# Optimization experiments

Measured on AMD Instinct MI355X. Metric: run time of the kernel, lower is better.

The kernel has to match this reference:

```python
import jax, jax.numpy as jnp
import numpy as np

N = 8192   # points
C = 64     # feature planes (planes[0])
H = 4      # num_heads
K = 16     # nsample (KNN neighbors)
DH = C // H
EPS = 1e-9


def setup_inputs() -> dict:
    key = jax.random.key(0)
    ks = jax.random.split(key, 13)
    w = lambda k, sh: jax.random.normal(k, sh, jnp.float32) * 0.05
    p = jax.random.normal(ks[0], (N, 3), jnp.float32)
    nrm = jax.random.normal(ks[1], (N, 3), jnp.float32)
    normals = nrm / jnp.sqrt(jnp.sum(nrm * nrm, -1, keepdims=True) + EPS)
    x = jax.random.normal(ks[2], (N, C), jnp.float32)
    return {
        "p": p, "x": x, "normals": normals,
        "Wq": w(ks[3], (C, C)), "Wk": w(ks[4], (C, C)), "Wv": w(ks[5], (C, C)),
        "Wo": w(ks[6], (C, C)),
        "ppf_w1": w(ks[7], (4, C)), "ppf_b1": jnp.zeros((C,), jnp.float32),
        "ppf_w2": w(ks[8], (C, C)), "ppf_b2": jnp.zeros((C,), jnp.float32),
        "ln_g": jnp.ones((C,), jnp.float32), "ln_b": jnp.zeros((C,), jnp.float32),
    }


def _angle(u, v):
    # rotation-invariant angle via atan2(||u x v||, u . v); eps keeps grads finite at 0
    cr = jnp.cross(u, v)
    return jnp.arctan2(jnp.sqrt(jnp.sum(cr * cr, -1) + EPS), jnp.sum(u * v, -1))


def reference(p, x, normals, Wq, Wk, Wv, Wo, ppf_w1, ppf_b1, ppf_w2, ppf_b2, ln_g, ln_b):
    # --- KNN grouping (pointops.queryandgroup equivalent) ---
    sq = jnp.sum(p * p, -1)
    d2 = sq[:, None] + sq[None, :] - 2.0 * (p @ p.T)   # (N,N) pairwise sq dists
    _, idx = jax.lax.top_k(-d2, K)                      # (N,K) neighbor indices

    # --- PPF features (calc_ppf_gpu) ---
    p_r = p[idx]                                        # (N,K,3)
    n_r = normals[idx]                                  # (N,K,3)
    d = p_r - p[:, None, :]
    nc = jnp.broadcast_to(normals[:, None, :], d.shape)
    ppf = jnp.stack([
        _angle(nc, d),
        _angle(n_r, d),
        _angle(nc, n_r),
        jnp.sqrt(jnp.sum(d * d, -1) + EPS),
    ], -1)                                              # (N,K,4)

    # --- LocalPPFTransformer: PPF-conditioned local multi-head attention ---
    pe = jax.nn.relu(ppf @ ppf_w1 + ppf_b1) @ ppf_w2 + ppf_b2   # (N,K,C)
    q = (x @ Wq).reshape(N, H, DH)
    xg = x[idx]                                                  # (N,K,C) gather
    k = (xg @ Wk + pe).reshape(N, K, H, DH)
    v = (xg @ Wv + pe).reshape(N, K, H, DH)
    scale = 1.0 / np.sqrt(DH).astype(np.float32)
    attn = jax.nn.softmax(jnp.einsum('nhd,nkhd->nhk', q, k) * scale, axis=-1)
    out = jnp.einsum('nhk,nkhd->nhd', attn, v).reshape(N, C) @ Wo

    # --- block tail: LayerNorm, residual, ReLU ---
    mu = jnp.mean(out, -1, keepdims=True)
    var = jnp.var(out, -1, keepdims=True)
    out = (out - mu) * jax.lax.rsqrt(var + 1e-5) * ln_g + ln_b
    return jax.nn.relu(out + x)
```

## Files before the change

kernel.cpp:

```cpp
#include <hip/hip_runtime.h>
#include <hip/hip_bf16.h>
#include <math.h>

#define N_PTS 8192
#define QPW 4
#define LCAP 192
#define KNN_BLOCKS (N_PTS / 4)

#define OFF_W2 0
#define OFF_WO 4096
#define OFF_WQB 8192
#define OFF_WKB 12288
#define OFF_WVB 16384
#define PACK_N 20480
#define PREP_BLOCKS (N_PTS / 256)
#define PACK_BLOCKS ((PACK_N + 255) / 256)

typedef __hip_bfloat16 bf16;
typedef __attribute__((ext_vector_type(8))) short short8;
typedef __attribute__((ext_vector_type(4))) float floatx4;

#define INFF __int_as_float(0x7f800000)

__device__ __forceinline__ float ldf(const float* p, int i) { return p[i]; }
__device__ __forceinline__ float ldf(const bf16* p, int i) { return __bfloat162float(p[i]); }
__device__ __forceinline__ void stf(float* p, int i, float v) { p[i] = v; }
__device__ __forceinline__ void stf(bf16* p, int i, float v) { p[i] = __float2bfloat16(v); }

__device__ __forceinline__ unsigned short f2bfbits(float x) {
    bf16 h = __float2bfloat16(x);
    return *reinterpret_cast<unsigned short*>(&h);
}
__device__ __forceinline__ float bfbits2f(unsigned short u) {
    bf16 h;
    *reinterpret_cast<unsigned short*>(&h) = u;
    return __bfloat162float(h);
}

__device__ __forceinline__ short8 load_xfrag(const bf16* x, int row, int off) {
    return *(const short8*)((const unsigned short*)x + row * 64 + off);
}
__device__ __forceinline__ short8 load_xfrag(const float* x, int row, int off) {
    short8 v;
#pragma unroll
    for (int i = 0; i < 8; ++i) v[i] = (short)f2bfbits(x[row * 64 + off + i]);
    return v;
}

__device__ __forceinline__ bool is_bf16(const void* g) {
    return *(const unsigned int*)g != 0x3F800000u;
}

template <typename T>
__device__ __forceinline__ void prep_pack_body(const T* p, float4* p4,
                                               const T* w2, const T* Wo,
                                               const T* Wq, const T* Wk,
                                               const T* Wv,
                                               unsigned short* pack) {
    if (blockIdx.x < PREP_BLOCKS) {
        int i = blockIdx.x * 256 + threadIdx.x;
        float x = ldf(p, 3 * i + 0);
        float y = ldf(p, 3 * i + 1);
        float z = ldf(p, 3 * i + 2);
        p4[i] = make_float4(x, y, z, 0.5f * (x * x + y * y + z * z));
        return;
    }
    int i = (blockIdx.x - PREP_BLOCKS) * 256 + threadIdx.x;
    if (i >= PACK_N) return;
    if (i >= OFF_WO && i < OFF_WQB) {
        int j = i - OFF_WO, t = j >> 6, c = j & 63;
        pack[i] = f2bfbits(ldf(Wo, c * 64 + t));
    } else {
        const T* W = (i < OFF_WO) ? w2
                     : (i < OFF_WKB ? Wq : (i < OFF_WVB ? Wk : Wv));
        int j = i & 4095;
        int ii = j & 7, lane = (j >> 3) & 63, frag = j >> 9;
        int tile = frag >> 1, s = frag & 1, g = lane >> 4, m16 = lane & 15;
        int k = s * 32 + g * 8 + ii, n = tile * 16 + m16;
        pack[i] = f2bfbits(ldf(W, k * 64 + n));
    }
}
__global__ __launch_bounds__(256) void prep_pack_kernel(
    const void* p, float4* p4, const void* w2, const void* Wo, const void* Wq,
    const void* Wk, const void* Wv, unsigned short* pack, const void* gref) {
    if (is_bf16(gref))
        prep_pack_body<bf16>((const bf16*)p, p4, (const bf16*)w2,
                             (const bf16*)Wo, (const bf16*)Wq, (const bf16*)Wk,
                             (const bf16*)Wv, pack);
    else
        prep_pack_body<float>((const float*)p, p4, (const float*)w2,
                              (const float*)Wo, (const float*)Wq,
                              (const float*)Wk, (const float*)Wv, pack);
}

__global__ __launch_bounds__(256, 8) void knn_kernel(
    const float4* __restrict__ p4, unsigned short* __restrict__ nbrs_g) {
    __shared__ unsigned long long list[QPW][LCAP];
    __shared__ float Tw_sh[QPW][4];
    __shared__ unsigned int cnt[QPW];
    __shared__ int nbrs[QPW][16];

    const int tid = threadIdx.x;
    const int lane = tid & 63;
    const int wave = tid >> 6;
    const int qbase = blockIdx.x * QPW;
    const int cbase = wave * (N_PTS / 4);

    float4 c[QPW];
#pragma unroll
    for (int q = 0; q < QPW; ++q) c[q] = p4[qbase + q];

    if (tid < QPW) cnt[tid] = 0;

    float lmin[QPW];
#pragma unroll
    for (int q = 0; q < QPW; ++q) lmin[q] = INFF;

#pragma unroll 4
    for (int it = 0; it < N_PTS / 4 / 64; ++it) {
        float4 pj = p4[cbase + it * 64 + lane];
#pragma unroll
        for (int q = 0; q < QPW; ++q) {
            float f = fmaf(-c[q].x, pj.x,
                      fmaf(-c[q].y, pj.y, fmaf(-c[q].z, pj.z, pj.w)));
            lmin[q] = fminf(lmin[q], f);
        }
    }

#pragma unroll
    for (int q = 0; q < QPW; ++q) {
        float v = lmin[q];
#pragma unroll
        for (int k = 2; k <= 64; k <<= 1) {
#pragma unroll
            for (int j = k >> 1; j >= 1; j >>= 1) {
                float o = __shfl_xor(v, j, 64);
                bool keepmin = (((lane & k) == 0) == ((lane & j) == 0));
                v = keepmin ? fminf(v, o) : fmaxf(v, o);
            }
        }
        float Tw = __shfl(v, 15, 64);
        if (lane == 0) Tw_sh[q][wave] = Tw;
    }
    __syncthreads();

    float T[QPW];
#pragma unroll
    for (int q = 0; q < QPW; ++q)
        T[q] = fminf(fminf(Tw_sh[q][0], Tw_sh[q][1]),
                     fminf(Tw_sh[q][2], Tw_sh[q][3]));

#pragma unroll 2
    for (int it = 0; it < N_PTS / 4 / 64; ++it) {
        int j = cbase + it * 64 + lane;
        float4 pj = p4[j];
#pragma unroll
        for (int q = 0; q < QPW; ++q) {
            float f = fmaf(-c[q].x, pj.x,
                      fmaf(-c[q].y, pj.y, fmaf(-c[q].z, pj.z, pj.w)));
            bool sel = f <= T[q];
            unsigned long long ball = __ballot(sel);
            if (ball) {
                int leader = (int)__ffsll((long long)ball) - 1;
                unsigned int base = 0;
                if (lane == leader)
                    base = atomicAdd(&cnt[q], (unsigned int)__popcll(ball));
                base = (unsigned int)__shfl((int)base, leader, 64);
                if (sel) {
                    unsigned int bits = __float_as_uint(f);
                    bits ^= (unsigned int)(((int)bits >> 31)) | 0x80000000u;
                    unsigned long long key =
                        ((unsigned long long)bits << 32) | (unsigned int)j;
                    unsigned int mb =
                        __builtin_amdgcn_mbcnt_lo((unsigned int)ball, 0u);
                    mb = __builtin_amdgcn_mbcnt_hi((unsigned int)(ball >> 32),
                                                   mb);
                    unsigned int pos = base + mb;
                    if (pos < LCAP) list[q][pos] = key;
                }
            }
        }
    }
    __syncthreads();

    {
        const int q = wave;
        int m = cnt[q] < (unsigned)LCAP ? (int)cnt[q] : LCAP;
#pragma unroll
        for (int s = 0; s < LCAP / 64; ++s) {
            int idx = lane + s * 64;
            if (idx < m) {
                unsigned long long k = list[q][idx];
                int r = 0;
#pragma unroll 1
                for (int e = 0; e < m; ++e) r += (list[q][e] < k);
                if (r < 16) nbrs[q][r] = (int)(k & 0xFFFFFFFFu);
            }
        }
    }
    __syncthreads();

    if (tid < QPW * 16)
        nbrs_g[qbase * 16 + tid] =
            (unsigned short)((const int*)nbrs)[tid];
}

__device__ __forceinline__ float angle3(float ux, float uy, float uz, float vx,
                                        float vy, float vz) {
    float cx = uy * vz - uz * vy;
    float cy = uz * vx - ux * vz;
    float cz = ux * vy - uy * vx;
    float cn = sqrtf(cx * cx + cy * cy + cz * cz + 1e-9f);
    float d = ux * vx + uy * vy + uz * vz;
    return atan2f(cn, d);
}

template <typename T>
__device__ __forceinline__ void attn4_body(
    int n, int t, const float4* p4, const T* normals, const T* w1, const T* b1,
    const T* b2, const unsigned short* pack, const T* x, const T* ln_g,
    const T* ln_b, T* out, const unsigned short* nbr, float* scr,
    unsigned short (*kh)[72], unsigned short (*vbuf)[72]) {
    const int m16 = t & 15, g = t >> 4;

    float w10 = ldf(w1, 0 * 64 + t);
    float w11 = ldf(w1, 1 * 64 + t);
    float w12 = ldf(w1, 2 * 64 + t);
    float w13 = ldf(w1, 3 * 64 + t);
    float bb1 = ldf(b1, t);
    float b2c[4];
#pragma unroll
    for (int tile = 0; tile < 4; ++tile) b2c[tile] = ldf(b2, tile * 16 + m16);

    {
        int k = t >> 2, f = t & 3;
        int j = nbr[k];
        float4 pc = p4[n];
        float4 pj = p4[j];
        float dx = pj.x - pc.x, dy = pj.y - pc.y, dz = pj.z - pc.z;
        float v;
        if (f == 3) {
            v = sqrtf(dx * dx + dy * dy + dz * dz + 1e-9f);
        } else if (f == 0) {
            float ncx = ldf(normals, n * 3 + 0);
            float ncy = ldf(normals, n * 3 + 1);
            float ncz = ldf(normals, n * 3 + 2);
            v = angle3(ncx, ncy, ncz, dx, dy, dz);
        } else if (f == 1) {
            float njx = ldf(normals, j * 3 + 0);
            float njy = ldf(normals, j * 3 + 1);
            float njz = ldf(normals, j * 3 + 2);
            v = angle3(njx, njy, njz, dx, dy, dz);
        } else {
            float ncx = ldf(normals, n * 3 + 0);
            float ncy = ldf(normals, n * 3 + 1);
            float ncz = ldf(normals, n * 3 + 2);
            float njx = ldf(normals, j * 3 + 0);
            float njy = ldf(normals, j * 3 + 1);
            float njz = ldf(normals, j * 3 + 2);
            v = angle3(ncx, ncy, ncz, njx, njy, njz);
        }
        scr[t] = v;
    }
    __syncthreads();

    {
        const float4* pp = (const float4*)scr;
#pragma unroll
        for (int k = 0; k < 16; ++k) {
            float4 pf = pp[k];
            float h = fmaf(pf.w, w13,
                      fmaf(pf.z, w12, fmaf(pf.y, w11, fmaf(pf.x, w10, bb1))));
            kh[k][t] = f2bfbits(fmaxf(h, 0.0f));
        }
    }
    __syncthreads();

    short8 afr[2];
#pragma unroll
    for (int s = 0; s < 2; ++s)
        afr[s] = *(const short8*)&kh[m16][g * 8 + s * 32];

    short8 axfr[2], qfr[2];
#pragma unroll
    for (int s = 0; s < 2; ++s) {
        axfr[s] = load_xfrag(x, nbr[m16], g * 8 + s * 32);
        qfr[s] = load_xfrag(x, n, g * 8 + s * 32);
    }

    float qreg = 0.f;
    {
        const short8* pw2 = (const short8*)(pack + OFF_W2);
        const short8* pwq = (const short8*)(pack + OFF_WQB);
        const short8* pwk = (const short8*)(pack + OFF_WKB);
        const short8* pwv = (const short8*)(pack + OFF_WVB);
#pragma unroll
        for (int tile = 0; tile < 4; ++tile) {
            floatx4 accp = (floatx4){0.f, 0.f, 0.f, 0.f};
            accp = __builtin_amdgcn_mfma_f32_16x16x32_bf16(
                afr[0], pw2[(tile * 2 + 0) * 64 + t], accp, 0, 0, 0);
            accp = __builtin_amdgcn_mfma_f32_16x16x32_bf16(
                afr[1], pw2[(tile * 2 + 1) * 64 + t], accp, 0, 0, 0);
            floatx4 acck = accp;
            acck = __builtin_amdgcn_mfma_f32_16x16x32_bf16(
                axfr[0], pwk[(tile * 2 + 0) * 64 + t], acck, 0, 0, 0);
            acck = __builtin_amdgcn_mfma_f32_16x16x32_bf16(
                axfr[1], pwk[(tile * 2 + 1) * 64 + t], acck, 0, 0, 0);
            floatx4 accv = accp;
            accv = __builtin_amdgcn_mfma_f32_16x16x32_bf16(
                axfr[0], pwv[(tile * 2 + 0) * 64 + t], accv, 0, 0, 0);
            accv = __builtin_amdgcn_mfma_f32_16x16x32_bf16(
                axfr[1], pwv[(tile * 2 + 1) * 64 + t], accv, 0, 0, 0);
            floatx4 accq = (floatx4){0.f, 0.f, 0.f, 0.f};
            accq = __builtin_amdgcn_mfma_f32_16x16x32_bf16(
                qfr[0], pwq[(tile * 2 + 0) * 64 + t], accq, 0, 0, 0);
            accq = __builtin_amdgcn_mfma_f32_16x16x32_bf16(
                qfr[1], pwq[(tile * 2 + 1) * 64 + t], accq, 0, 0, 0);
            if (tile == g) qreg = accq[0];
#pragma unroll
            for (int r = 0; r < 4; ++r) {
                kh[g * 4 + r][tile * 16 + m16] =
                    f2bfbits(acck[r] + b2c[tile]);
                vbuf[g * 4 + r][tile * 16 + m16] =
                    f2bfbits(accv[r] + b2c[tile]);
            }
        }
    }
    __syncthreads();

    int h = t >> 4, kk = t & 15;
    float s = 0.f;
    {
        const short8* kv = (const short8*)&kh[kk][h * 16];
        short8 k0 = kv[0], k1 = kv[1];
        int qb = t & 0x30;
#pragma unroll
        for (int i = 0; i < 8; ++i)
            s = fmaf(__shfl(qreg, qb + i, 64),
                     bfbits2f((unsigned short)k0[i]), s);
#pragma unroll
        for (int i = 0; i < 8; ++i)
            s = fmaf(__shfl(qreg, qb + 8 + i, 64),
                     bfbits2f((unsigned short)k1[i]), s);
    }
    s *= 0.25f;

    float m = s;
#pragma unroll
    for (int off = 1; off < 16; off <<= 1)
        m = fmaxf(m, __shfl_xor(m, off, 16));
    float e = expf(s - m);
    float sum = e;
#pragma unroll
    for (int off = 1; off < 16; off <<= 1) sum += __shfl_xor(sum, off, 16);
    scr[t] = e / sum;
    __syncthreads();

    int hh = t >> 4;
    float o = 0.f;
    {
        const float4* aw = (const float4*)&scr[hh * 16];
#pragma unroll
        for (int j = 0; j < 4; ++j) {
            float4 a = aw[j];
            o = fmaf(a.x, bfbits2f(vbuf[j * 4 + 0][t]), o);
            o = fmaf(a.y, bfbits2f(vbuf[j * 4 + 1][t]), o);
            o = fmaf(a.z, bfbits2f(vbuf[j * 4 + 2][t]), o);
            o = fmaf(a.w, bfbits2f(vbuf[j * 4 + 3][t]), o);
        }
    }
    __syncthreads();
    scr[t] = o;
    __syncthreads();

    float wo = 0.f;
    {
        const short8* wo8 = (const short8*)(pack + OFF_WO) + t * 8;
        const float4* av = (const float4*)scr;
#pragma unroll
        for (int c8 = 0; c8 < 8; ++c8) {
            short8 w = wo8[c8];
            float4 a0 = av[c8 * 2 + 0], a1 = av[c8 * 2 + 1];
            wo = fmaf(a0.x, bfbits2f((unsigned short)w[0]), wo);
            wo = fmaf(a0.y, bfbits2f((unsigned short)w[1]), wo);
            wo = fmaf(a0.z, bfbits2f((unsigned short)w[2]), wo);
            wo = fmaf(a0.w, bfbits2f((unsigned short)w[3]), wo);
            wo = fmaf(a1.x, bfbits2f((unsigned short)w[4]), wo);
            wo = fmaf(a1.y, bfbits2f((unsigned short)w[5]), wo);
            wo = fmaf(a1.z, bfbits2f((unsigned short)w[6]), wo);
            wo = fmaf(a1.w, bfbits2f((unsigned short)w[7]), wo);
        }
    }

    float sum2 = wo;
#pragma unroll
    for (int off = 1; off < 64; off <<= 1) sum2 += __shfl_xor(sum2, off, 64);
    float mu = sum2 * (1.0f / 64.0f);
    float dc = wo - mu;
    float vs = dc * dc;
#pragma unroll
    for (int off = 1; off < 64; off <<= 1) vs += __shfl_xor(vs, off, 64);
    float var = vs * (1.0f / 64.0f);

    float y = dc * rsqrtf(var + 1e-5f) * ldf(ln_g, t) + ldf(ln_b, t);
    float r = y + ldf(x, n * 64 + t);
    stf(out, n * 64 + t, fmaxf(r, 0.0f));
}

__global__ __launch_bounds__(256, 8) void attn_kernel(
    const float4* __restrict__ p4, const void* normals, const void* w1,
    const void* b1, const void* b2, const unsigned short* __restrict__ pack,
    const void* x, const void* ln_g, const void* ln_b,
    const unsigned short* __restrict__ nbrs_g, void* out) {
    __shared__ __align__(16) unsigned short kh4[4][16][72];
    __shared__ __align__(16) unsigned short vbuf4[4][16][72];
    __shared__ __align__(16) float scratch4[4][64];

    const int lane = threadIdx.x & 63;
    const int wave = threadIdx.x >> 6;
    const int n = blockIdx.x * QPW + wave;
    const unsigned short* nbr = nbrs_g + n * 16;

    if (is_bf16(ln_g))
        attn4_body<bf16>(n, lane, p4, (const bf16*)normals, (const bf16*)w1,
                         (const bf16*)b1, (const bf16*)b2, pack,
                         (const bf16*)x, (const bf16*)ln_g, (const bf16*)ln_b,
                         (bf16*)out, nbr, scratch4[wave], kh4[wave],
                         vbuf4[wave]);
    else
        attn4_body<float>(n, lane, p4, (const float*)normals, (const float*)w1,
                          (const float*)b1, (const float*)b2, pack,
                          (const float*)x, (const float*)ln_g,
                          (const float*)ln_b, (float*)out, nbr,
                          scratch4[wave], kh4[wave], vbuf4[wave]);
}

extern "C" void kernel_launch(void* const* d_in, const int* in_sizes, int n_in,
                              void* d_out, int out_size, void* d_ws, size_t ws_size,
                              hipStream_t stream) {
    const void* p   = d_in[0];
    const void* x   = d_in[1];
    const void* nrm = d_in[2];
    const void* Wq  = d_in[3];
    const void* Wk  = d_in[4];
    const void* Wv  = d_in[5];
    const void* Wo  = d_in[6];
    const void* w1  = d_in[7];
    const void* b1  = d_in[8];
    const void* w2  = d_in[9];
    const void* b2  = d_in[10];
    const void* g   = d_in[11];
    const void* b   = d_in[12];

    char* ws = (char*)d_ws;
    float4* p4 = (float4*)ws;  ws += (size_t)N_PTS * sizeof(float4);
    unsigned short* pack = (unsigned short*)ws;  ws += PACK_N * 2;
    unsigned short* nbrs_g = (unsigned short*)ws;  ws += (size_t)N_PTS * 16 * 2;

    prep_pack_kernel<<<PREP_BLOCKS + PACK_BLOCKS, 256, 0, stream>>>(
        p, p4, w2, Wo, Wq, Wk, Wv, pack, g);
    knn_kernel<<<KNN_BLOCKS, 256, 0, stream>>>(p4, nbrs_g);
    attn_kernel<<<KNN_BLOCKS, 256, 0, stream>>>(p4, nrm, w1, b1, b2, pack, x,
                                                g, b, nbrs_g, d_out);
}
```

Baseline: 155.7 us.

## Use SoA point layout and packed FP32 FMA in KNN distance scans

```diff
diff --git a/kernel.cpp b/kernel.cpp
--- a/kernel.cpp
+++ b/kernel.cpp
@@ -19,8 +19,21 @@
 typedef __hip_bfloat16 bf16;
 typedef __attribute__((ext_vector_type(8))) short short8;
 typedef __attribute__((ext_vector_type(4))) float floatx4;
+typedef __attribute__((ext_vector_type(2))) float floatx2;
 
 #define INFF __int_as_float(0x7f800000)
+
+__device__ __forceinline__ floatx2 pk_fma(floatx2 a, floatx2 b, floatx2 c) {
+    floatx2 d;
+    asm("v_pk_fma_f32 %0, %1, %2, %3" : "=v"(d) : "v"(a), "v"(b), "v"(c));
+    return d;
+}
+__device__ __forceinline__ floatx2 min2(floatx2 a, floatx2 b) {
+    floatx2 r;
+    r.x = fminf(a.x, b.x);
+    r.y = fminf(a.y, b.y);
+    return r;
+}
 
 __device__ __forceinline__ float ldf(const float* p, int i) { return p[i]; }
 __device__ __forceinline__ float ldf(const bf16* p, int i) { return __bfloat162float(p[i]); }
@@ -53,16 +66,22 @@
 
 template <typename T>
 __device__ __forceinline__ void prep_pack_body(const T* p, float4* p4,
-                                               const T* w2, const T* Wo,
-                                               const T* Wq, const T* Wk,
-                                               const T* Wv,
+                                               float* sx, float* sy, float* sz,
+                                               float* sw, const T* w2,
+                                               const T* Wo, const T* Wq,
+                                               const T* Wk, const T* Wv,
                                                unsigned short* pack) {
     if (blockIdx.x < PREP_BLOCKS) {
         int i = blockIdx.x * 256 + threadIdx.x;
         float x = ldf(p, 3 * i + 0);
         float y = ldf(p, 3 * i + 1);
         float z = ldf(p, 3 * i + 2);
-        p4[i] = make_float4(x, y, z, 0.5f * (x * x + y * y + z * z));
+        float w = 0.5f * (x * x + y * y + z * z);
+        p4[i] = make_float4(x, y, z, w);
+        sx[i] = x;
+        sy[i] = y;
+        sz[i] = z;
+        sw[i] = w;
         return;
     }
     int i = (blockIdx.x - PREP_BLOCKS) * 256 + threadIdx.x;
@@ -81,20 +100,24 @@
     }
 }
 __global__ __launch_bounds__(256) void prep_pack_kernel(
-    const void* p, float4* p4, const void* w2, const void* Wo, const void* Wq,
-    const void* Wk, const void* Wv, unsigned short* pack, const void* gref) {
+    const void* p, float4* p4, float* sx, float* sy, float* sz, float* sw,
+    const void* w2, const void* Wo, const void* Wq, const void* Wk,
+    const void* Wv, unsigned short* pack, const void* gref) {
     if (is_bf16(gref))
-        prep_pack_body<bf16>((const bf16*)p, p4, (const bf16*)w2,
-                             (const bf16*)Wo, (const bf16*)Wq, (const bf16*)Wk,
-                             (const bf16*)Wv, pack);
+        prep_pack_body<bf16>((const bf16*)p, p4, sx, sy, sz, sw,
+                             (const bf16*)w2, (const bf16*)Wo, (const bf16*)Wq,
+                             (const bf16*)Wk, (const bf16*)Wv, pack);
     else
-        prep_pack_body<float>((const float*)p, p4, (const float*)w2,
-                              (const float*)Wo, (const float*)Wq,
-                              (const float*)Wk, (const float*)Wv, pack);
+        prep_pack_body<float>((const float*)p, p4, sx, sy, sz, sw,
+                              (const float*)w2, (const float*)Wo,
+                              (const float*)Wq, (const float*)Wk,
+                              (const float*)Wv, pack);
 }
 
 __global__ __launch_bounds__(256, 8) void knn_kernel(
-    const float4* __restrict__ p4, unsigned short* __restrict__ nbrs_g) {
+    const float4* __restrict__ p4, const float* __restrict__ sx,
+    const float* __restrict__ sy, const float* __restrict__ sz,
+    const float* __restrict__ sw, unsigned short* __restrict__ nbrs_g) {
     __shared__ unsigned long long list[QPW][LCAP];
     __shared__ float Tw_sh[QPW][4];
     __shared__ unsigned int cnt[QPW];
@@ -106,30 +129,45 @@
     const int qbase = blockIdx.x * QPW;
     const int cbase = wave * (N_PTS / 4);
 
-    float4 c[QPW];
-#pragma unroll
-    for (int q = 0; q < QPW; ++q) c[q] = p4[qbase + q];
+    floatx2 ncx[QPW], ncy[QPW], ncz[QPW];
+#pragma unroll
+    for (int q = 0; q < QPW; ++q) {
+        float4 c = p4[qbase + q];
+        ncx[q] = (floatx2){-c.x, -c.x};
+        ncy[q] = (floatx2){-c.y, -c.y};
+        ncz[q] = (floatx2){-c.z, -c.z};
+    }
 
     if (tid < QPW) cnt[tid] = 0;
 
-    float lmin[QPW];
-#pragma unroll
-    for (int q = 0; q < QPW; ++q) lmin[q] = INFF;
-
-#pragma unroll 4
-    for (int it = 0; it < N_PTS / 4 / 64; ++it) {
-        float4 pj = p4[cbase + it * 64 + lane];
+    floatx2 lmin2[QPW];
+#pragma unroll
+    for (int q = 0; q < QPW; ++q) lmin2[q] = (floatx2){INFF, INFF};
+
+#pragma unroll 1
+    for (int it = 0; it < N_PTS / 4 / 256; ++it) {
+        int base = cbase + it * 256 + lane * 4;
+        float4 x4 = *(const float4*)&sx[base];
+        float4 y4 = *(const float4*)&sy[base];
+        float4 z4 = *(const float4*)&sz[base];
+        float4 w4 = *(const float4*)&sw[base];
+        floatx2 xlo = (floatx2){x4.x, x4.y}, xhi = (floatx2){x4.z, x4.w};
+        floatx2 ylo = (floatx2){y4.x, y4.y}, yhi = (floatx2){y4.z, y4.w};
+        floatx2 zlo = (floatx2){z4.x, z4.y}, zhi = (floatx2){z4.z, z4.w};
+        floatx2 wlo = (floatx2){w4.x, w4.y}, whi = (floatx2){w4.z, w4.w};
 #pragma unroll
         for (int q = 0; q < QPW; ++q) {
-            float f = fmaf(-c[q].x, pj.x,
-                      fmaf(-c[q].y, pj.y, fmaf(-c[q].z, pj.z, pj.w)));
-            lmin[q] = fminf(lmin[q], f);
+            floatx2 flo = pk_fma(ncx[q], xlo,
+                          pk_fma(ncy[q], ylo, pk_fma(ncz[q], zlo, wlo)));
+            floatx2 fhi = pk_fma(ncx[q], xhi,
+                          pk_fma(ncy[q], yhi, pk_fma(ncz[q], zhi, whi)));
+            lmin2[q] = min2(lmin2[q], min2(flo, fhi));
         }
     }
 
 #pragma unroll
     for (int q = 0; q < QPW; ++q) {
-        float v = lmin[q];
+        float v = fminf(lmin2[q].x, lmin2[q].y);
 #pragma unroll
         for (int k = 2; k <= 64; k <<= 1) {
 #pragma unroll
@@ -150,33 +188,49 @@
         T[q] = fminf(fminf(Tw_sh[q][0], Tw_sh[q][1]),
                      fminf(Tw_sh[q][2], Tw_sh[q][3]));
 
-#pragma unroll 2
-    for (int it = 0; it < N_PTS / 4 / 64; ++it) {
-        int j = cbase + it * 64 + lane;
-        float4 pj = p4[j];
+#pragma unroll 1
+    for (int it = 0; it < N_PTS / 4 / 256; ++it) {
+        int base = cbase + it * 256 + lane * 4;
+        float4 x4 = *(const float4*)&sx[base];
+        float4 y4 = *(const float4*)&sy[base];
+        float4 z4 = *(const float4*)&sz[base];
+        float4 w4 = *(const float4*)&sw[base];
+        floatx2 xlo = (floatx2){x4.x, x4.y}, xhi = (floatx2){x4.z, x4.w};
+        floatx2 ylo = (floatx2){y4.x, y4.y}, yhi = (floatx2){y4.z, y4.w};
+        floatx2 zlo = (floatx2){z4.x, z4.y}, zhi = (floatx2){z4.z, z4.w};
+        floatx2 wlo = (floatx2){w4.x, w4.y}, whi = (floatx2){w4.z, w4.w};
 #pragma unroll
         for (int q = 0; q < QPW; ++q) {
-            float f = fmaf(-c[q].x, pj.x,
-                      fmaf(-c[q].y, pj.y, fmaf(-c[q].z, pj.z, pj.w)));
-            bool sel = f <= T[q];
-            unsigned long long ball = __ballot(sel);
-            if (ball) {
-                int leader = (int)__ffsll((long long)ball) - 1;
-                unsigned int base = 0;
-                if (lane == leader)
-                    base = atomicAdd(&cnt[q], (unsigned int)__popcll(ball));
-                base = (unsigned int)__shfl((int)base, leader, 64);
-                if (sel) {
-                    unsigned int bits = __float_as_uint(f);
-                    bits ^= (unsigned int)(((int)bits >> 31)) | 0x80000000u;
-                    unsigned long long key =
-                        ((unsigned long long)bits << 32) | (unsigned int)j;
-                    unsigned int mb =
-                        __builtin_amdgcn_mbcnt_lo((unsigned int)ball, 0u);
-                    mb = __builtin_amdgcn_mbcnt_hi((unsigned int)(ball >> 32),
-                                                   mb);
-                    unsigned int pos = base + mb;
-                    if (pos < LCAP) list[q][pos] = key;
+            floatx2 flo = pk_fma(ncx[q], xlo,
+                          pk_fma(ncy[q], ylo, pk_fma(ncz[q], zlo, wlo)));
+            floatx2 fhi = pk_fma(ncx[q], xhi,
+                          pk_fma(ncy[q], yhi, pk_fma(ncz[q], zhi, whi)));
+            float fs0 = flo.x, fs1 = flo.y, fs2 = fhi.x, fs3 = fhi.y;
+#pragma unroll
+            for (int s = 0; s < 4; ++s) {
+                float f = (s == 0) ? fs0 : (s == 1) ? fs1 : (s == 2) ? fs2
+                                                                     : fs3;
+                bool sel = f <= T[q];
+                unsigned long long ball = __ballot(sel);
+                if (ball) {
+                    int leader = (int)__ffsll((long long)ball) - 1;
+                    unsigned int b0 = 0;
+                    if (lane == leader)
+                        b0 = atomicAdd(&cnt[q], (unsigned int)__popcll(ball));
+                    b0 = (unsigned int)__shfl((int)b0, leader, 64);
+                    if (sel) {
+                        unsigned int bits = __float_as_uint(f);
+                        bits ^= (unsigned int)(((int)bits >> 31)) | 0x80000000u;
+                        unsigned long long key =
+                            ((unsigned long long)bits << 32) |
+                            (unsigned int)(base + s);
+                        unsigned int mb =
+                            __builtin_amdgcn_mbcnt_lo((unsigned int)ball, 0u);
+                        mb = __builtin_amdgcn_mbcnt_hi(
+                            (unsigned int)(ball >> 32), mb);
+                        unsigned int pos = b0 + mb;
+                        if (pos < LCAP) list[q][pos] = key;
+                    }
                 }
             }
         }
@@ -456,10 +510,14 @@
     float4* p4 = (float4*)ws;  ws += (size_t)N_PTS * sizeof(float4);
     unsigned short* pack = (unsigned short*)ws;  ws += PACK_N * 2;
     unsigned short* nbrs_g = (unsigned short*)ws;  ws += (size_t)N_PTS * 16 * 2;
+    float* sx = (float*)ws;  ws += (size_t)N_PTS * 4;
+    float* sy = (float*)ws;  ws += (size_t)N_PTS * 4;
+    float* sz = (float*)ws;  ws += (size_t)N_PTS * 4;
+    float* sw = (float*)ws;  ws += (size_t)N_PTS * 4;
 
     prep_pack_kernel<<<PREP_BLOCKS + PACK_BLOCKS, 256, 0, stream>>>(
-        p, p4, w2, Wo, Wq, Wk, Wv, pack, g);
-    knn_kernel<<<KNN_BLOCKS, 256, 0, stream>>>(p4, nbrs_g);
+        p, p4, sx, sy, sz, sw, w2, Wo, Wq, Wk, Wv, pack, g);
+    knn_kernel<<<KNN_BLOCKS, 256, 0, stream>>>(p4, sx, sy, sz, sw, nbrs_g);
     attn_kernel<<<KNN_BLOCKS, 256, 0, stream>>>(p4, nrm, w1, b1, b2, pack, x,
                                                 g, b, nbrs_g, d_out);
 }
```

Result: slower. 162.4 us (+4.3%).
